# Performance work log

Hardware: AMD Instinct MI355X
Metric: run time of the kernel (lower is better)

## Reference

```python
import jax, jax.numpy as jnp
import numpy as np

B, C, IMG, P = 32, 3, 224, 16
E, HEADS, L, NC = 768, 8, 6, 1000
HD = E // HEADS            # 96
NP = (IMG // P) ** 2       # 196 patches
N = NP + 1                 # +cls
SCALE = HD ** -0.5
EPS = 1e-5


def layer_norm(x, g, b):
    m = jnp.mean(x, axis=-1, keepdims=True)
    v = jnp.mean(jnp.square(x - m), axis=-1, keepdims=True)
    return (x - m) * jax.lax.rsqrt(v + EPS) * g + b


def _forward(x, conv_w, conv_b, cls_token, pos_emb,
             qkv_w, qkv_b, proj_w, proj_b, ln1_g, ln1_b,
             mlp_w1, mlp_b1, mlp_w2, mlp_b2, ln2_g, ln2_b,
             head_ln_g, head_ln_b, head_w, head_b):
    b = x.shape[0]
    h = IMG // P
    # patch embed: conv with kernel==stride == non-overlapping patch matmul
    xp = x.reshape(b, C, h, P, h, P)                       # b c h i w j
    x = jnp.einsum('bchiwj,ecij->bhwe', xp, conv_w) + conv_b
    x = x.reshape(b, NP, E)
    # cls token + positional embedding (broadcast add, as in torch source)
    cls = jnp.broadcast_to(cls_token[None], (b, 1, E))
    x = jnp.concatenate([cls, x], axis=1) + pos_emb        # [b, N, E]

    def block(x, p):
        qw, qb, pw, pb, g1, b1, w1, bb1, w2, bb2, g2, b2 = p
        # --- attention sublayer (post-norm residual) ---
        qkv = x @ qw.T + qb                                # [b, N, 3E]
        qkv = qkv.reshape(b, N, 3, HEADS, HD)
        qkv = jnp.transpose(qkv, (2, 0, 3, 1, 4))          # [3, b, H, N, d]
        q, k, v = qkv[0], qkv[1], qkv[2]
        sim = jnp.einsum('bhqd,bhkd->bhqk', q, k)
        sim = jax.nn.softmax(sim, axis=-1) * SCALE         # scale AFTER softmax (faithful)
        att = jnp.einsum('bhnk,bhkd->bhnd', sim, v)
        att = jnp.transpose(att, (0, 2, 1, 3)).reshape(b, N, E)
        att = att @ pw.T + pb
        x = layer_norm(x + att, g1, b1)
        # --- MLP sublayer (post-norm residual) ---
        hdn = jax.nn.gelu(x @ w1.T + bb1, approximate=False)
        mlp = hdn @ w2.T + bb2
        x = layer_norm(x + mlp, g2, b2)
        return x, None

    x, _ = jax.lax.scan(block, x, (qkv_w, qkv_b, proj_w, proj_b,
                                   ln1_g, ln1_b, mlp_w1, mlp_b1,
                                   mlp_w2, mlp_b2, ln2_g, ln2_b))
    # classifier: mean pool -> LN -> Linear
    x = jnp.mean(x, axis=1)
    x = layer_norm(x, head_ln_g, head_ln_b)
    return x @ head_w.T + head_b


def setup_inputs() -> dict:
    key = jax.random.key(0)
    ks = jax.random.split(key, 24)
    s = 0.02
    FF = 4 * E
    return {
        'x': jax.random.normal(ks[0], (B, C, IMG, IMG), jnp.float32),
        'conv_w': jax.random.normal(ks[1], (E, C, P, P), jnp.float32) * s,
        'conv_b': jnp.zeros((E,), jnp.float32),
        'cls_token': jax.random.uniform(ks[2], (1, E), jnp.float32),
        'pos_emb': jax.random.uniform(ks[3], (N, E), jnp.float32),
        'qkv_w': jax.random.normal(ks[4], (L, 3 * E, E), jnp.float32) * s,
        'qkv_b': jnp.zeros((L, 3 * E), jnp.float32),
        'proj_w': jax.random.normal(ks[5], (L, E, E), jnp.float32) * s,
        'proj_b': jnp.zeros((L, E), jnp.float32),
        'ln1_g': jnp.ones((L, E), jnp.float32),
        'ln1_b': jnp.zeros((L, E), jnp.float32),
        'mlp_w1': jax.random.normal(ks[6], (L, FF, E), jnp.float32) * s,
        'mlp_b1': jnp.zeros((L, FF), jnp.float32),
        'mlp_w2': jax.random.normal(ks[7], (L, E, FF), jnp.float32) * s,
        'mlp_b2': jnp.zeros((L, E), jnp.float32),
        'ln2_g': jnp.ones((L, E), jnp.float32),
        'ln2_b': jnp.zeros((L, E), jnp.float32),
        'head_ln_g': jnp.ones((E,), jnp.float32),
        'head_ln_b': jnp.zeros((E,), jnp.float32),
        'head_w': jax.random.normal(ks[8], (NC, E), jnp.float32) * s,
        'head_b': jnp.zeros((NC,), jnp.float32),
    }


def reference(x, conv_w, conv_b, cls_token, pos_emb,
              qkv_w, qkv_b, proj_w, proj_b, ln1_g, ln1_b,
              mlp_w1, mlp_b1, mlp_w2, mlp_b2, ln2_g, ln2_b,
              head_ln_g, head_ln_b, head_w, head_b):
    return _forward(x, conv_w, conv_b, cls_token, pos_emb,
                    qkv_w, qkv_b, proj_w, proj_b, ln1_g, ln1_b,
                    mlp_w1, mlp_b1, mlp_w2, mlp_b2, ln2_g, ln2_b,
                    head_ln_g, head_ln_b, head_w, head_b)
```

## Files before the change

kernel.cpp:

```cpp
#include <hip/hip_runtime.h>
#include <hip/hip_bf16.h>
#include <math.h>

constexpr int Bsz = 32, Cch = 3, IMGS = 224, PP = 16;
constexpr int E = 768, HEADS = 8, Lnum = 6, NC = 1000;
constexpr int HD = 96;
constexpr int NP = 196;
constexpr int Nn = 197;
constexpr int FF = 3072;
constexpr float SCALE = 0.10206207261596575f;
constexpr float EPSc  = 1e-5f;

using short8 = __attribute__((ext_vector_type(8))) short;
using f32x4  = __attribute__((ext_vector_type(4))) float;

__device__ __forceinline__ void async_cp16(const void* g, void* l) {
    __builtin_amdgcn_global_load_lds((const __attribute__((address_space(1))) void*)g,
                                     (__attribute__((address_space(3))) void*)l, 16, 0, 0);
}

__global__ void f2b_k(const float* __restrict__ in, __hip_bfloat16* __restrict__ out, int n4) {
    int i = blockIdx.x * 256 + threadIdx.x;
    if (i >= n4) return;
    const float4 v = ((const float4*)in)[i];
    size_t o = (size_t)i * 4;
    out[o + 0] = __float2bfloat16(v.x);
    out[o + 1] = __float2bfloat16(v.y);
    out[o + 2] = __float2bfloat16(v.z);
    out[o + 3] = __float2bfloat16(v.w);
}

__global__ void f2b4_k(const float* __restrict__ s0, const float* __restrict__ s1,
                       const float* __restrict__ s2, const float* __restrict__ s3,
                       __hip_bfloat16* __restrict__ d0, __hip_bfloat16* __restrict__ d1,
                       __hip_bfloat16* __restrict__ d2, __hip_bfloat16* __restrict__ d3,
                       int n0, int n1, int n2, int n3) {
    int i = blockIdx.x * 256 + threadIdx.x;
    const float* s; __hip_bfloat16* d; int base;
    if (i < n0)                { s = s0; d = d0; base = 0; }
    else if (i < n0 + n1)      { s = s1; d = d1; base = n0; }
    else if (i < n0 + n1 + n2) { s = s2; d = d2; base = n0 + n1; }
    else if (i < n0 + n1 + n2 + n3) { s = s3; d = d3; base = n0 + n1 + n2; }
    else return;
    int k = i - base;
    const float4 v = ((const float4*)s)[k];
    size_t o = (size_t)k * 4;
    d[o + 0] = __float2bfloat16(v.x);
    d[o + 1] = __float2bfloat16(v.y);
    d[o + 2] = __float2bfloat16(v.z);
    d[o + 3] = __float2bfloat16(v.w);
}

__global__ void im2col_k(const float* __restrict__ x, __hip_bfloat16* __restrict__ A) {
    int idx = blockIdx.x * 256 + threadIdx.x;
    if (idx >= Bsz * NP * (Cch * PP * PP)) return;
    int col = idx % 768;
    int row = idx / 768;
    int b  = row / NP;
    int p  = row % NP;
    int hh = p / 14, ww = p % 14;
    int c  = col / 256;
    int rem = col % 256;
    int i = rem / 16, j = rem % 16;
    A[idx] = __float2bfloat16(
        x[(((size_t)b * Cch + c) * IMGS + hh * 16 + i) * IMGS + ww * 16 + j]);
}

template <int TM, int OUT_BF16, int ACT, int AHEADS>
__global__ __launch_bounds__(256, 4) void gemm_bf16_k(
    const __hip_bfloat16* __restrict__ A, const __hip_bfloat16* __restrict__ W,
    const float* __restrict__ bias, void* __restrict__ outp,
    int M, int N, int K)
{
    constexpr int NA = TM / 64;
    constexpr int JN = (TM == 128) ? 4 : 2;
    __shared__ char As[2][TM * 64];
    __shared__ char Bs[2][8192];
    const int tid  = threadIdx.x;
    const int lane = tid & 63;
    const int w    = tid >> 6;

    const int GX = (int)gridDim.x, GY = (int)gridDim.y;
    const int nb  = GX * GY;
    const int lin = (int)blockIdx.x + GX * (int)blockIdx.y;
    const int qq  = nb >> 3, rr = nb & 7;
    const int xcd = lin & 7, j8 = lin >> 3;
    const int s   = (xcd < rr ? xcd * (qq + 1) : rr * (qq + 1) + (xcd - rr) * qq) + j8;
    const int bx  = s / GY;
    const int by  = s - bx * GY;
    const int m0 = bx * TM, n0 = by * 128;
    const int wm = (TM == 128) ? (w & 1) * 64 : 0;
    const int wn = (TM == 128) ? (w >> 1) * 64 : w * 32;

    const __hip_bfloat16* agv[NA];
    int abv[NA], acv[NA];
#pragma unroll
    for (int i = 0; i < NA; i++) {
        int q = tid + i * 256;
        int r = q >> 2;
        int c = (q & 3) ^ ((r >> 1) & 3);
        int am = m0 + r; if (am > M - 1) am = M - 1;
        if (AHEADS == 0) {
            agv[i] = A + (size_t)am * K + c * 8;
            abv[i] = 0; acv[i] = 0;
        } else {
            int b_ = am / 197, i_ = am - b_ * 197;
            abv[i] = b_ * 8 * 18912 + i_ * 96;
            acv[i] = c;
            agv[i] = A;
        }
    }
    const int q0 = tid, q1 = tid + 256;
    const int rb0 = q0 >> 2, rb1 = q1 >> 2;
    const int cb0 = (q0 & 3) ^ ((rb0 >> 1) & 3);
    const int cb1 = (q1 & 3) ^ ((rb1 >> 1) & 3);
    const __hip_bfloat16* bg0 = W + (size_t)(n0 + rb0) * K + cb0 * 8;
    const __hip_bfloat16* bg1 = W + (size_t)(n0 + rb1) * K + cb1 * 8;
    char* const asd0 = As[0] + w * 1024;
    char* const asd1 = As[1] + w * 1024;
    char* const bsd0 = Bs[0] + w * 1024;
    char* const bsd1 = Bs[1] + w * 1024;

    const int frow = lane & 15, fquad = lane >> 4;
    const int swz = (fquad ^ ((frow >> 1) & 3)) * 16;
    const char* const ar0 = As[0] + (wm + frow) * 64 + swz;
    const char* const ar1 = As[1] + (wm + frow) * 64 + swz;
    const char* const br0 = Bs[0] + (wn + frow) * 64 + swz;
    const char* const br1 = Bs[1] + (wn + frow) * 64 + swz;

    f32x4 acc[4][JN] = {};

#define STAGE(k0_, asd_, bsd_)                                                \
    {                                                                         \
        _Pragma("unroll")                                                     \
        for (int i_ = 0; i_ < NA; i_++) {                                     \
            if (AHEADS == 0) {                                                \
                async_cp16(agv[i_] + (k0_), (asd_) + i_ * 4096);              \
            } else {                                                          \
                int kc_ = acv[i_] + ((k0_) >> 3);                             \
                int h_ = kc_ / 12, dd_ = kc_ - h_ * 12;                       \
                async_cp16(agv[i_] + abv[i_] + h_ * 18912 + dd_ * 8,          \
                           (asd_) + i_ * 4096);                               \
            }                                                                 \
        }                                                                     \
        async_cp16(bg0 + (k0_), (bsd_));                                      \
        async_cp16(bg1 + (k0_), (bsd_) + 4096);                               \
    }

#define WAIT_N()                                                              \
    {                                                                         \
        if constexpr (TM == 128) asm volatile("s_waitcnt vmcnt(4)" ::: "memory"); \
        else                     asm volatile("s_waitcnt vmcnt(3)" ::: "memory"); \
    }

#define FENCE_BAR()                                                           \
    {                                                                         \
        __builtin_amdgcn_sched_barrier(0);                                    \
        __builtin_amdgcn_s_barrier();                                         \
        __builtin_amdgcn_sched_barrier(0);                                    \
    }

#define COMPUTE(arp_, brp_)                                                   \
    {                                                                         \
        short8 af[4], bf[JN];                                                 \
        _Pragma("unroll")                                                     \
        for (int i_ = 0; i_ < 4; i_++) af[i_] = *(const short8*)((arp_) + i_ * 1024); \
        _Pragma("unroll")                                                     \
        for (int j_ = 0; j_ < JN; j_++) bf[j_] = *(const short8*)((brp_) + j_ * 1024); \
        _Pragma("unroll")                                                     \
        for (int i_ = 0; i_ < 4; i_++)                                        \
            _Pragma("unroll")                                                 \
            for (int j_ = 0; j_ < JN; j_++)                                   \
                acc[i_][j_] = __builtin_amdgcn_mfma_f32_16x16x32_bf16(af[i_], bf[j_], acc[i_][j_], 0, 0, 0); \
    }

    const int kiters = K / 32;
    STAGE(0, asd0, bsd0);
#pragma unroll 1
    for (int it = 0; it < kiters; it += 2) {
        STAGE((it + 1) * 32, asd1, bsd1);
        WAIT_N();
        FENCE_BAR();
        COMPUTE(ar0, br0);
        FENCE_BAR();
        if (it + 2 < kiters) {
            STAGE((it + 2) * 32, asd0, bsd0);
            WAIT_N();
        } else {
            asm volatile("s_waitcnt vmcnt(0)" ::: "memory");
        }
        FENCE_BAR();
        COMPUTE(ar1, br1);
        if (it + 2 < kiters) FENCE_BAR();
    }
#undef STAGE
#undef WAIT_N
#undef FENCE_BAR
#undef COMPUTE

#pragma unroll
    for (int i = 0; i < 4; i++) {
#pragma unroll
        for (int j = 0; j < JN; j++) {
#pragma unroll
            for (int r = 0; r < 4; r++) {
                int row = m0 + wm + i * 16 + fquad * 4 + r;
                int col = n0 + wn + j * 16 + frow;
                if (row < M) {
                    float v = acc[i][j][r] + bias[col];
                    if (ACT == 1) v = 0.5f * v * (1.0f + erff(v * 0.70710678118654752f));
                    if (OUT_BF16) ((__hip_bfloat16*)outp)[(size_t)row * N + col] = __float2bfloat16(v);
                    else          ((float*)outp)[(size_t)row * N + col] = v;
                }
            }
        }
    }
}

__global__ void assemble_k(const float* __restrict__ ptmp, const float* __restrict__ cls,
                           const float* __restrict__ pos, float* __restrict__ X,
                           __hip_bfloat16* __restrict__ Xb) {
    int idx = blockIdx.x * 256 + threadIdx.x;
    if (idx >= Bsz * Nn * E) return;
    int e = idx % E;
    int r = idx / E;
    int n = r % Nn, b = r / Nn;
    float v = (n == 0) ? cls[e] : ptmp[((size_t)b * NP + (n - 1)) * E + e];
    v += pos[(size_t)n * E + e];
    X[idx] = v;
    Xb[idx] = __float2bfloat16(v);
}

__global__ void vtr_k(const __hip_bfloat16* __restrict__ qkv, __hip_bfloat16* __restrict__ Vtg) {
    __shared__ short T[64][104];
    const int tid = threadIdx.x;
    const int bh = blockIdx.y, jc = blockIdx.x;
    const int b = bh >> 3, h = bh & 7;
    const int j0 = jc * 64;
#pragma unroll
    for (int it = 0; it < 3; it++) {
        int idx = it * 256 + tid;
        int jl = idx / 12, off = (idx % 12) * 8;
        int j = j0 + jl;
        short8 v = {0, 0, 0, 0, 0, 0, 0, 0};
        if (j <= 196)
            v = *(const short8*)(qkv + (size_t)(b * Nn + j) * 2304 + 1536 + h * 96 + off);
        *(short8*)(&T[jl][off]) = v;
    }
    __syncthreads();
#pragma unroll
    for (int it = 0; it < 3; it++) {
        int idx = it * 256 + tid;
        int d = idx >> 3, c = idx & 7;
        int col = j0 + c * 8;
        if (col < 232) {
            short8 v;
#pragma unroll
            for (int k = 0; k < 8; k++) v[k] = T[c * 8 + k][d];
            *(short8*)(Vtg + ((size_t)bh * 96 + d) * 232 + col) = v;
        }
    }
}

__global__ __launch_bounds__(256, 1) void fattn_k(
    const __hip_bfloat16* __restrict__ qkv,
    const __hip_bfloat16* __restrict__ Vtg,
    __hip_bfloat16* __restrict__ atth)
{
    __shared__ __align__(16) char SL[44544 + 4 * 1280];
    char* const Ps = SL + 44544;
    const int tid = threadIdx.x, lane = tid & 63, w = tid >> 6;
    const int bh = blockIdx.x & 255;
    const int g  = blockIdx.x >> 8;
    const int tbase  = g * 7;
    const int ntiles = g ? 6 : 7;
    const int b = bh >> 3, h = bh & 7;
    const int frow = lane & 15, quad = lane >> 4;

#pragma unroll
    for (int it = 0; it < 10; it++) {
        int c = it * 256 + tid;
        if (c < 197 * 12) {
            int j = c / 12, cc = c % 12;
            short8 v = *(const short8*)(qkv + ((size_t)(b * 197 + j)) * 2304 + 768 + h * 96 + cc * 8);
            *(short8*)(SL + j * 208 + cc * 16) = v;
        }
    }
    __syncthreads();

    short8 pf[2][7];
#pragma unroll 1
    for (int t = 0; t < 2; t++) {
        const int ml = w + 4 * t;
        if (ml >= ntiles) break;
        const int mt = tbase + ml;
        const int qi = min(mt * 16 + frow, 196);
        const __hip_bfloat16* qrow = qkv + ((size_t)(b * 197 + qi)) * 2304 + h * 96 + quad * 8;
        short8 qf[3];
#pragma unroll
        for (int kc = 0; kc < 3; kc++) qf[kc] = *(const short8*)(qrow + kc * 32);

        f32x4 sacc[13];
#pragma unroll
        for (int nt = 0; nt < 13; nt++) sacc[nt] = (f32x4){0.f, 0.f, 0.f, 0.f};
#pragma unroll
        for (int nt = 0; nt < 13; nt++) {
#pragma unroll
            for (int kc = 0; kc < 3; kc++) {
                short8 kf = *(const short8*)(SL + (nt * 16 + frow) * 208 + (kc * 32 + quad * 8) * 2);
                sacc[nt] = __builtin_amdgcn_mfma_f32_16x16x32_bf16(qf[kc], kf, sacc[nt], 0, 0, 0);
            }
        }

        float mx[4] = {-1e30f, -1e30f, -1e30f, -1e30f};
#pragma unroll
        for (int nt = 0; nt < 13; nt++) {
            bool masked = (nt == 12) && (frow >= 5);
#pragma unroll
            for (int r = 0; r < 4; r++) {
                float v = masked ? -1e30f : sacc[nt][r];
                sacc[nt][r] = v;
                mx[r] = fmaxf(mx[r], v);
            }
        }
#pragma unroll
        for (int m = 1; m <= 8; m <<= 1)
#pragma unroll
            for (int r = 0; r < 4; r++) mx[r] = fmaxf(mx[r], __shfl_xor(mx[r], m));
        float sm[4] = {0.f, 0.f, 0.f, 0.f};
#pragma unroll
        for (int nt = 0; nt < 13; nt++) {
            bool masked = (nt == 12) && (frow >= 5);
#pragma unroll
            for (int r = 0; r < 4; r++) {
                float e = masked ? 0.f : __expf(sacc[nt][r] - mx[r]);
                sacc[nt][r] = e;
                sm[r] += e;
            }
        }
#pragma unroll
        for (int m = 1; m <= 8; m <<= 1)
#pragma unroll
            for (int r = 0; r < 4; r++) sm[r] += __shfl_xor(sm[r], m);
        float inv[4];
#pragma unroll
        for (int r = 0; r < 4; r++) inv[r] = SCALE / sm[r];

        char* const myPs = Ps + w * 1280;
#pragma unroll
        for (int kc = 0; kc < 7; kc++) {
#pragma unroll
            for (int tt = 0; tt < 2; tt++) {
                int t2 = kc * 2 + tt;
#pragma unroll
                for (int r = 0; r < 4; r++) {
                    float pv = (t2 < 13) ? sacc[t2][r] * inv[r] : 0.f;
                    *(__hip_bfloat16*)(myPs + (quad * 4 + r) * 80 + (tt * 16 + frow) * 2) =
                        __float2bfloat16(pv);
                }
            }
            pf[t][kc] = *(const short8*)(myPs + frow * 80 + quad * 16);
        }
    }
    __syncthreads();

    {
        const char* src = (const char*)(Vtg + (size_t)bh * 96 * 232);
#pragma unroll
        for (int i = 0; i < 11; i++) {
            int c = i * 256 + w * 64 + lane;
            if (c < 96 * 29)
                async_cp16(src + (size_t)c * 16, SL + (size_t)(i * 256 + w * 64) * 16);
        }
    }
    __syncthreads();

#pragma unroll 1
    for (int t = 0; t < 2; t++) {
        const int ml = w + 4 * t;
        if (ml >= ntiles) break;
        const int mt = tbase + ml;
        f32x4 oacc[6];
#pragma unroll
        for (int dt = 0; dt < 6; dt++) oacc[dt] = (f32x4){0.f, 0.f, 0.f, 0.f};
#pragma unroll
        for (int kc = 0; kc < 7; kc++) {
#pragma unroll
            for (int dt = 0; dt < 6; dt++) {
                short8 vf = *(const short8*)(SL + (size_t)(dt * 16 + frow) * 464 +
                                             (kc * 32 + quad * 8) * 2);
                oacc[dt] = __builtin_amdgcn_mfma_f32_16x16x32_bf16(pf[t][kc], vf, oacc[dt], 0, 0, 0);
            }
        }
#pragma unroll
        for (int dt = 0; dt < 6; dt++)
#pragma unroll
            for (int r = 0; r < 4; r++) {
                int i = mt * 16 + quad * 4 + r;
                if (i < 197)
                    atth[((size_t)bh * 197 + i) * 96 + dt * 16 + frow] =
                        __float2bfloat16(oacc[dt][r]);
            }
    }
}

__global__ void add_ln_k(float* __restrict__ X, const float* __restrict__ T,
                         const float* __restrict__ g, const float* __restrict__ bb,
                         __hip_bfloat16* __restrict__ Xb) {
    const size_t row = blockIdx.x;
    float* xr = X + row * E;
    const float* tr = T + row * E;
    const int t = threadIdx.x;
    __shared__ float red[4];
    float v[3];
    float s = 0.f;
#pragma unroll
    for (int i = 0; i < 3; i++) {
        v[i] = xr[t + i * 256] + tr[t + i * 256];
        s += v[i];
    }
    for (int off = 32; off > 0; off >>= 1) s += __shfl_down(s, off);
    int wid = t >> 6, lane = t & 63;
    if (lane == 0) red[wid] = s;
    __syncthreads();
    if (t == 0) red[0] = red[0] + red[1] + red[2] + red[3];
    __syncthreads();
    float mean = red[0] / 768.f;
    __syncthreads();
    float s2 = 0.f;
#pragma unroll
    for (int i = 0; i < 3; i++) {
        float dl = v[i] - mean;
        s2 += dl * dl;
    }
    for (int off = 32; off > 0; off >>= 1) s2 += __shfl_down(s2, off);
    if (lane == 0) red[wid] = s2;
    __syncthreads();
    if (t == 0) red[0] = red[0] + red[1] + red[2] + red[3];
    __syncthreads();
    float rs = rsqrtf(red[0] / 768.f + EPSc);
#pragma unroll
    for (int i = 0; i < 3; i++) {
        int e = t + i * 256;
        float o = (v[i] - mean) * rs * g[e] + bb[e];
        xr[e] = o;
        Xb[row * E + e] = __float2bfloat16(o);
    }
}

__global__ void pool_part_k(const float* __restrict__ X, float* __restrict__ part) {
    const int b = blockIdx.x, c = blockIdx.y, t = threadIdx.x;
    const int n0 = c * 28;
    const int n1 = (c == 6) ? Nn : n0 + 28;
    float a0 = 0.f, a1 = 0.f, a2 = 0.f;
    for (int n = n0; n < n1; n++) {
        const float* r = X + ((size_t)(b * Nn + n)) * E;
        a0 += r[t];
        a1 += r[t + 256];
        a2 += r[t + 512];
    }
    float* o = part + ((size_t)(b * 7 + c)) * E;
    o[t] = a0;
    o[t + 256] = a1;
    o[t + 512] = a2;
}

__global__ void pool_fin_k(const float* __restrict__ part, const float* __restrict__ g,
                           const float* __restrict__ bb, float* __restrict__ pooled) {
    __shared__ float red[4];
    const int b = blockIdx.x, t = threadIdx.x;
    float loc[3];
#pragma unroll
    for (int i = 0; i < 3; i++) {
        int e = t + i * 256;
        float s = 0.f;
#pragma unroll
        for (int c = 0; c < 7; c++) s += part[((size_t)(b * 7 + c)) * E + e];
        loc[i] = s / (float)Nn;
    }
    float s = loc[0] + loc[1] + loc[2];
    for (int off = 32; off > 0; off >>= 1) s += __shfl_down(s, off);
    int wid = t >> 6, lane = t & 63;
    if (lane == 0) red[wid] = s;
    __syncthreads();
    if (t == 0) red[0] = red[0] + red[1] + red[2] + red[3];
    __syncthreads();
    float mean = red[0] / 768.f;
    __syncthreads();
    float s2 = 0.f;
#pragma unroll
    for (int i = 0; i < 3; i++) {
        float dl = loc[i] - mean;
        s2 += dl * dl;
    }
    for (int off = 32; off > 0; off >>= 1) s2 += __shfl_down(s2, off);
    if (lane == 0) red[wid] = s2;
    __syncthreads();
    if (t == 0) red[0] = red[0] + red[1] + red[2] + red[3];
    __syncthreads();
    float rs = rsqrtf(red[0] / 768.f + EPSc);
#pragma unroll
    for (int i = 0; i < 3; i++) {
        int e = t + i * 256;
        pooled[(size_t)b * E + e] = (loc[i] - mean) * rs * g[e] + bb[e];
    }
}

__global__ void head_k(const float* __restrict__ pooled, const float* __restrict__ hw,
                       const float* __restrict__ hb, float* __restrict__ out) {
    __shared__ float ps[768];
    const int b = blockIdx.y;
    const int s = blockIdx.x;
    const int t = threadIdx.x, lane = t & 63, w = t >> 6;
    for (int e = t; e < 768; e += 256) ps[e] = pooled[(size_t)b * E + e];
    __syncthreads();
    float pl[12];
#pragma unroll
    for (int j = 0; j < 12; j++) pl[j] = ps[j * 64 + lane];
    for (int i = 0; i < 10; i++) {
        int o = s * 40 + w * 10 + i;
        const float* wr = hw + (size_t)o * 768;
        float acc = 0.f;
#pragma unroll
        for (int j = 0; j < 12; j++) acc += pl[j] * wr[j * 64 + lane];
        for (int off = 32; off > 0; off >>= 1) acc += __shfl_down(acc, off);
        if (lane == 0) out[(size_t)b * NC + o] = acc + hb[o];
    }
}

extern "C" void kernel_launch(void* const* d_in, const int* in_sizes, int n_in,
                              void* d_out, int out_size, void* d_ws, size_t ws_size,
                              hipStream_t stream) {
    const float* x        = (const float*)d_in[0];
    const float* conv_w   = (const float*)d_in[1];
    const float* conv_b   = (const float*)d_in[2];
    const float* cls_tok  = (const float*)d_in[3];
    const float* pos_emb  = (const float*)d_in[4];
    const float* qkv_w    = (const float*)d_in[5];
    const float* qkv_b    = (const float*)d_in[6];
    const float* proj_w   = (const float*)d_in[7];
    const float* proj_b   = (const float*)d_in[8];
    const float* ln1_g    = (const float*)d_in[9];
    const float* ln1_b    = (const float*)d_in[10];
    const float* mlp_w1   = (const float*)d_in[11];
    const float* mlp_b1   = (const float*)d_in[12];
    const float* mlp_w2   = (const float*)d_in[13];
    const float* mlp_b2   = (const float*)d_in[14];
    const float* ln2_g    = (const float*)d_in[15];
    const float* ln2_b    = (const float*)d_in[16];
    const float* hln_g    = (const float*)d_in[17];
    const float* hln_b    = (const float*)d_in[18];
    const float* head_w   = (const float*)d_in[19];
    const float* head_b   = (const float*)d_in[20];
    float* out = (float*)d_out;

    const int M = Bsz * Nn;

    char* p = (char*)d_ws;
    __hip_bfloat16* Xb   = (__hip_bfloat16*)p;  p += (size_t)M * E * 2;
    float*          X    = (float*)p;           p += (size_t)M * E * 4;
    __hip_bfloat16* qwb  = (__hip_bfloat16*)p;  p += (size_t)3 * E * E * 2;
    __hip_bfloat16* pwb  = (__hip_bfloat16*)p;  p += (size_t)E * E * 2;
    __hip_bfloat16* w1b  = (__hip_bfloat16*)p;  p += (size_t)FF * E * 2;
    __hip_bfloat16* w2b  = (__hip_bfloat16*)p;  p += (size_t)E * FF * 2;
    __hip_bfloat16* cwb  = (__hip_bfloat16*)p;  p += (size_t)E * E * 2;
    __hip_bfloat16* atth = (__hip_bfloat16*)p;  p += (size_t)M * E * 2;
    float*          pool = (float*)p;           p += (size_t)Bsz * E * 4;
    char* R = p;
    __hip_bfloat16* qkvb = (__hip_bfloat16*)R;
    __hip_bfloat16* Vtg  = (__hip_bfloat16*)(R + 29048832);
    __hip_bfloat16* Hb   = (__hip_bfloat16*)R;
    float*          Ctmp = (float*)(R + 40452096);
    __hip_bfloat16* imb  = (__hip_bfloat16*)R;

    {
        f2b_k<<<(E * E / 4 + 255) / 256, 256, 0, stream>>>(conv_w, cwb, E * E / 4);
        int tot = Bsz * NP * 768;
        im2col_k<<<(tot + 255) / 256, 256, 0, stream>>>(x, imb);
        dim3 g(98, 6);
        gemm_bf16_k<64, 0, 0, 0><<<g, 256, 0, stream>>>(imb, cwb, conv_b, Ctmp, Bsz * NP, E, E);
        int tot2 = Bsz * Nn * E;
        assemble_k<<<(tot2 + 255) / 256, 256, 0, stream>>>(Ctmp, cls_tok, pos_emb, X, Xb);
    }

    const int MB128 = (M + 127) / 128;
    const int MB64  = (M + 63) / 64;
    const int cn0 = 3 * E * E / 4, cn1 = E * E / 4, cn2 = FF * E / 4, cn3 = E * FF / 4;
    const int cgrid = (cn0 + cn1 + cn2 + cn3 + 255) / 256;

    for (int l = 0; l < Lnum; l++) {
        const float* qw = qkv_w + (size_t)l * 3 * E * E;
        const float* qb = qkv_b + (size_t)l * 3 * E;
        const float* pw = proj_w + (size_t)l * E * E;
        const float* pb = proj_b + (size_t)l * E;
        const float* g1 = ln1_g + (size_t)l * E;
        const float* b1 = ln1_b + (size_t)l * E;
        const float* w1 = mlp_w1 + (size_t)l * FF * E;
        const float* bb1 = mlp_b1 + (size_t)l * FF;
        const float* w2 = mlp_w2 + (size_t)l * E * FF;
        const float* bb2 = mlp_b2 + (size_t)l * E;
        const float* g2 = ln2_g + (size_t)l * E;
        const float* b2 = ln2_b + (size_t)l * E;

        f2b4_k<<<cgrid, 256, 0, stream>>>(qw, pw, w1, w2, qwb, pwb, w1b, w2b,
                                          cn0, cn1, cn2, cn3);

        gemm_bf16_k<128, 1, 0, 0><<<dim3(MB128, 18), 256, 0, stream>>>(Xb, qwb, qb, qkvb, M, 3 * E, E);
        vtr_k<<<dim3(4, Bsz * HEADS), 256, 0, stream>>>(qkvb, Vtg);
        fattn_k<<<Bsz * HEADS * 2, 256, 0, stream>>>(qkvb, Vtg, atth);
        gemm_bf16_k<64, 0, 0, 1><<<dim3(MB64, 6), 256, 0, stream>>>(atth, pwb, pb, Ctmp, M, E, E);
        add_ln_k<<<M, 256, 0, stream>>>(X, Ctmp, g1, b1, Xb);
        gemm_bf16_k<128, 1, 1, 0><<<dim3(MB128, 24), 256, 0, stream>>>(Xb, w1b, bb1, Hb, M, FF, E);
        gemm_bf16_k<64, 0, 0, 0><<<dim3(MB64, 6), 256, 0, stream>>>(Hb, w2b, bb2, Ctmp, M, E, FF);
        add_ln_k<<<M, 256, 0, stream>>>(X, Ctmp, g2, b2, Xb);
    }

    pool_part_k<<<dim3(Bsz, 7), 256, 0, stream>>>(X, Ctmp);
    pool_fin_k<<<Bsz, 256, 0, stream>>>(Ctmp, hln_g, hln_b, pool);
    head_k<<<dim3(25, Bsz), 256, 0, stream>>>(pool, head_w, head_b, out);
}
```

Before: 1.791 ms.

## Triple-buffer the bf16 GEMM k-loop and prefetch two stages ahead

```diff
diff --git a/kernel.cpp b/kernel.cpp
--- a/kernel.cpp
+++ b/kernel.cpp
@@ -67,15 +67,16 @@
 }
 
 template <int TM, int OUT_BF16, int ACT, int AHEADS>
-__global__ __launch_bounds__(256, 4) void gemm_bf16_k(
+__global__ __launch_bounds__(256, (TM == 128) ? 3 : 4) void gemm_bf16_k(
     const __hip_bfloat16* __restrict__ A, const __hip_bfloat16* __restrict__ W,
     const float* __restrict__ bias, void* __restrict__ outp,
     int M, int N, int K)
 {
     constexpr int NA = TM / 64;
     constexpr int JN = (TM == 128) ? 4 : 2;
-    __shared__ char As[2][TM * 64];
-    __shared__ char Bs[2][8192];
+    constexpr int NLOADS = NA + 2;
+    __shared__ char As[3][TM * 64];
+    __shared__ char Bs[3][8192];
     const int tid  = threadIdx.x;
     const int lane = tid & 63;
     const int w    = tid >> 6;
@@ -118,15 +119,19 @@
     const __hip_bfloat16* bg1 = W + (size_t)(n0 + rb1) * K + cb1 * 8;
     char* const asd0 = As[0] + w * 1024;
     char* const asd1 = As[1] + w * 1024;
+    char* const asd2 = As[2] + w * 1024;
     char* const bsd0 = Bs[0] + w * 1024;
     char* const bsd1 = Bs[1] + w * 1024;
+    char* const bsd2 = Bs[2] + w * 1024;
 
     const int frow = lane & 15, fquad = lane >> 4;
     const int swz = (fquad ^ ((frow >> 1) & 3)) * 16;
     const char* const ar0 = As[0] + (wm + frow) * 64 + swz;
     const char* const ar1 = As[1] + (wm + frow) * 64 + swz;
+    const char* const ar2 = As[2] + (wm + frow) * 64 + swz;
     const char* const br0 = Bs[0] + (wn + frow) * 64 + swz;
     const char* const br1 = Bs[1] + (wn + frow) * 64 + swz;
+    const char* const br2 = Bs[2] + (wn + frow) * 64 + swz;
 
     f32x4 acc[4][JN] = {};
 
@@ -147,12 +152,6 @@
         async_cp16(bg1 + (k0_), (bsd_) + 4096);                               \
     }
 
-#define WAIT_N()                                                              \
-    {                                                                         \
-        if constexpr (TM == 128) asm volatile("s_waitcnt vmcnt(4)" ::: "memory"); \
-        else                     asm volatile("s_waitcnt vmcnt(3)" ::: "memory"); \
-    }
-
 #define FENCE_BAR()                                                           \
     {                                                                         \
         __builtin_amdgcn_sched_barrier(0);                                    \
@@ -174,29 +173,31 @@
                 acc[i_][j_] = __builtin_amdgcn_mfma_f32_16x16x32_bf16(af[i_], bf[j_], acc[i_][j_], 0, 0, 0); \
     }
 
+#define PHASE(toff_, arp_, brp_, asd_, bsd_)                                  \
+    {                                                                         \
+        if (it + (toff_) == kiters - 1) {                                     \
+            asm volatile("s_waitcnt vmcnt(0)" ::: "memory");                  \
+        } else {                                                              \
+            asm volatile("s_waitcnt vmcnt(%0)" :: "i"(NLOADS) : "memory");    \
+        }                                                                     \
+        FENCE_BAR();                                                          \
+        if (it + (toff_) + 2 < kiters) STAGE((it + (toff_) + 2) * 32, asd_, bsd_); \
+        COMPUTE(arp_, brp_);                                                  \
+    }
+
     const int kiters = K / 32;
     STAGE(0, asd0, bsd0);
+    STAGE(32, asd1, bsd1);
 #pragma unroll 1
-    for (int it = 0; it < kiters; it += 2) {
-        STAGE((it + 1) * 32, asd1, bsd1);
-        WAIT_N();
-        FENCE_BAR();
-        COMPUTE(ar0, br0);
-        FENCE_BAR();
-        if (it + 2 < kiters) {
-            STAGE((it + 2) * 32, asd0, bsd0);
-            WAIT_N();
-        } else {
-            asm volatile("s_waitcnt vmcnt(0)" ::: "memory");
-        }
-        FENCE_BAR();
-        COMPUTE(ar1, br1);
-        if (it + 2 < kiters) FENCE_BAR();
+    for (int it = 0; it < kiters; it += 3) {
+        PHASE(0, ar0, br0, asd2, bsd2);
+        PHASE(1, ar1, br1, asd0, bsd0);
+        PHASE(2, ar2, br2, asd1, bsd1);
     }
 #undef STAGE
-#undef WAIT_N
 #undef FENCE_BAR
 #undef COMPUTE
+#undef PHASE
 
 #pragma unroll
     for (int i = 0; i < 4; i++) {
```

Result: slower. 1.856 ms (+3.6%).
